# Performance work log

Measured on AMD Instinct MI355X. Metric: run time of the kernel, lower is better.

The kernel has to match this reference:

```python
import jax, jax.numpy as jnp
import numpy as np

N, Z, E, M0, M1, D = 16384, 100, 400, 4000, 2000, 4


def setup_inputs() -> dict:
    key = jax.random.key(0)
    k = jax.random.split(key, 7)
    return {
        "theta": jax.random.normal(k[0], (N, Z), jnp.float32),
        "alpha0": jax.random.normal(k[1], (M0, E), jnp.float32),
        "alpha1": jax.random.normal(k[2], (M1, E), jnp.float32),
        "beta": jax.random.normal(k[3], (Z, E), jnp.float32),
        "bias0": jax.random.normal(k[4], (D, M0), jnp.float32),
        "bias1": jax.random.normal(k[5], (D, M1), jnp.float32),
        "domain_idx": jax.random.randint(k[6], (N,), 0, D, dtype=jnp.int32),
    }


def _recon_mod(theta, alpha, beta, bias, domain_idx):
    # Topic_mod = (alpha @ beta.T).T == beta @ alpha.T : (Z, M)
    topic = beta @ alpha.T
    # per-domain GEMM + indexed bias-add + log_softmax + scatter-back
    # == single GEMM with per-row gathered bias (all domains present)
    logits = theta @ topic + bias[domain_idx]  # (N, M)
    return jax.nn.log_softmax(logits, axis=-1)


def reference(theta, alpha0, alpha1, beta, bias0, bias1, domain_idx):
    r0 = _recon_mod(theta, alpha0, beta, bias0, domain_idx)
    r1 = _recon_mod(theta, alpha1, beta, bias1, domain_idx)
    return (r0, r1)
```

## Files before the change

### kernel.cpp

```cpp
#include <hip/hip_runtime.h>
#include <hip/hip_bf16.h>

#define PN 16384
#define PZ 100
#define PE 400
#define PM0 4000
#define PM1 2000
#define KP 128
#define SEG1ROW 4096
#define MROWS 6144

typedef __attribute__((ext_vector_type(8))) _Float16 half8v;
typedef __attribute__((ext_vector_type(4))) float floatx4;
typedef __attribute__((ext_vector_type(4))) unsigned int uint4v;

__global__ __launch_bounds__(256) void fill_kernel(uint4v* __restrict__ p, int n16)
{
    int i = blockIdx.x * 256 + threadIdx.x;
    if (i < n16) p[i] = (uint4v){0u, 0u, 0u, 0u};
}

__global__ __launch_bounds__(256) void topic_kernel(
    const float* __restrict__ alpha0, const float* __restrict__ alpha1,
    const float* __restrict__ beta, _Float16* __restrict__ b2t)
{
    __shared__ float sAl[64][101];
    __shared__ float sBt[20][100];

    const int seg = (blockIdx.x >= 64);
    const int tile = seg ? (blockIdx.x - 64) : blockIdx.x;
    const float* alpha = seg ? alpha1 : alpha0;
    const int Mse = seg ? PM1 : PM0;
    const int rowbase = (seg ? SEG1ROW : 0) + tile * 64;
    const int m0 = tile * 64;

    const int tid = threadIdx.x;
    const int ml = tid & 63;
    const int zt = tid >> 6;
    const int z0 = blockIdx.y * 20;

    float acc[5] = {0.f, 0.f, 0.f, 0.f, 0.f};

    for (int ec = 0; ec < 4; ++ec) {
        #pragma unroll
        for (int l = 0; l < 25; ++l) {
            int idx = tid + l * 256;
            int mr = idx / 100;
            int e  = idx - mr * 100;
            int mm = m0 + mr;
            sAl[mr][e] = (mm < Mse) ? alpha[(size_t)mm * PE + ec * 100 + e] : 0.f;
        }
        for (int idx = tid; idx < 2000; idx += 256) {
            int zr = idx / 100;
            int e  = idx - zr * 100;
            sBt[zr][e] = beta[(size_t)(z0 + zr) * PE + ec * 100 + e];
        }
        __syncthreads();

        #pragma unroll 2
        for (int e = 0; e < 100; ++e) {
            float a = sAl[ml][e];
            #pragma unroll
            for (int zi = 0; zi < 5; ++zi)
                acc[zi] = fmaf(sBt[zt * 5 + zi][e], a, acc[zi]);
        }
        __syncthreads();
    }

    int m = m0 + ml;
    if (m < Mse) {
        #pragma unroll
        for (int zi = 0; zi < 5; ++zi)
            b2t[(size_t)(rowbase + ml) * KP + (z0 + zt * 5 + zi)] = (_Float16)acc[zi];
    }
}

__global__ __launch_bounds__(256) void bias_kernel(
    const float* __restrict__ bias0, const float* __restrict__ bias1,
    _Float16* __restrict__ b2t)
{
    int row = blockIdx.x * 256 + threadIdx.x;
    if (row >= MROWS) return;
    int seg = (row >= SEG1ROW);
    int m = row - (seg ? SEG1ROW : 0);
    int Mse = seg ? PM1 : PM0;
    const float* bias = seg ? bias1 : bias0;
    if (m < Mse) {
        #pragma unroll
        for (int d = 0; d < 4; ++d)
            b2t[(size_t)row * KP + 100 + d] = (_Float16)bias[(size_t)d * Mse + m];
    }
}

__global__ __launch_bounds__(512, 4) void fused_kernel(
    const float* __restrict__ theta,
    const _Float16* __restrict__ B2T,
    const int* __restrict__ dom,
    float* __restrict__ out0, float* __restrict__ out1)
{
    __shared__ __align__(1024) char sA[32 * 256];
    __shared__ float smx[8][32];
    __shared__ float sms[8][32];
    __shared__ float slse[32];

    const int tid = threadIdx.x;
    const int w   = tid >> 6;
    const int ll  = tid & 63;
    const int g   = ll >> 4;
    const int c   = ll & 15;
    const int n0  = blockIdx.x * 32;

    {
        int row  = tid >> 4;
        int slot = tid & 15;
        const float* tr = theta + (size_t)(n0 + row) * PZ + slot * 8;
        half8v h = (half8v)(_Float16)0.f;
        if (slot < 12) {
            float4 lo = *(const float4*)tr;
            float4 hi = *(const float4*)(tr + 4);
            h[0] = (_Float16)lo.x; h[1] = (_Float16)lo.y;
            h[2] = (_Float16)lo.z; h[3] = (_Float16)lo.w;
            h[4] = (_Float16)hi.x; h[5] = (_Float16)hi.y;
            h[6] = (_Float16)hi.z; h[7] = (_Float16)hi.w;
        } else if (slot == 12) {
            float4 lo = *(const float4*)tr;
            h[0] = (_Float16)lo.x; h[1] = (_Float16)lo.y;
            h[2] = (_Float16)lo.z; h[3] = (_Float16)lo.w;
            int d = dom[n0 + row];
            h[4] = (_Float16)(d == 0 ? 1.f : 0.f);
            h[5] = (_Float16)(d == 1 ? 1.f : 0.f);
            h[6] = (_Float16)(d == 2 ? 1.f : 0.f);
            h[7] = (_Float16)(d == 3 ? 1.f : 0.f);
        }
        *(half8v*)(sA + row * 256 + ((slot ^ (row & 7)) * 16)) = h;
    }
    __syncthreads();

    half8v aF[2][4];
    #pragma unroll
    for (int mi = 0; mi < 2; ++mi) {
        int row = mi * 16 + c;
        #pragma unroll
        for (int kb = 0; kb < 4; ++kb) {
            int slot = (kb * 4 + g) ^ (row & 7);
            aF[mi][kb] = *(const half8v*)(sA + row * 256 + slot * 16);
        }
    }

    const int mbase = w * 16 + c;

    for (int seg = 0; seg < 2; ++seg) {
        const int Mse = seg ? PM1 : PM0;
        const int NT  = seg ? 16 : 32;
        const _Float16* Bseg = B2T + (size_t)(seg ? SEG1ROW : 0) * KP;
        float* out = seg ? out1 : out0;

        const _Float16* bp0 = Bseg + (size_t)mbase * KP;
        const size_t TSTEP = (size_t)128 * KP;

        float mx_[2][4], sm_[2][4];
        #pragma unroll
        for (int mi = 0; mi < 2; ++mi)
            #pragma unroll
            for (int i = 0; i < 4; ++i) { mx_[mi][i] = -3.0e38f; sm_[mi][i] = 0.f; }

        auto loadB = [&](half8v (&bf)[4], const _Float16* p) {
            #pragma unroll
            for (int kb = 0; kb < 4; ++kb)
                bf[kb] = *(const half8v*)(p + kb * 32 + g * 8);
        };
        auto mfma8 = [&](half8v (&bf)[4], floatx4& a0, floatx4& a1) {
            a0 = (floatx4){0.f, 0.f, 0.f, 0.f};
            a1 = (floatx4){0.f, 0.f, 0.f, 0.f};
            #pragma unroll
            for (int kb = 0; kb < 4; ++kb) {
                a0 = __builtin_amdgcn_mfma_f32_16x16x32_f16(aF[0][kb], bf[kb], a0, 0, 0, 0);
                a1 = __builtin_amdgcn_mfma_f32_16x16x32_f16(aF[1][kb], bf[kb], a1, 0, 0, 0);
            }
        };
        auto stats_step = [&](floatx4& a0, floatx4& a1, int t) {
            const bool mv = (t * 128 + mbase) < Mse;
            float vv[2][4];
            float gm = -3.0e38f;
            #pragma unroll
            for (int mi = 0; mi < 2; ++mi)
                #pragma unroll
                for (int i = 0; i < 4; ++i) {
                    float v = mv ? (mi ? a1[i] : a0[i]) : -1.0e30f;
                    vv[mi][i] = v;
                    gm = fmaxf(gm, v - mx_[mi][i]);
                }
            if (gm <= 8.0f) {
                #pragma unroll
                for (int mi = 0; mi < 2; ++mi)
                    #pragma unroll
                    for (int i = 0; i < 4; ++i)
                        sm_[mi][i] += __expf(vv[mi][i] - mx_[mi][i]);
            } else {
                #pragma unroll
                for (int mi = 0; mi < 2; ++mi)
                    #pragma unroll
                    for (int i = 0; i < 4; ++i) {
                        float v  = vv[mi][i];
                        float nm = fmaxf(mx_[mi][i], v);
                        sm_[mi][i] = sm_[mi][i] * __expf(mx_[mi][i] - nm) + __expf(v - nm);
                        mx_[mi][i] = nm;
                    }
            }
        };

        {
            half8v bA[4], bB[4];
            floatx4 a0, a1;
            const _Float16* bp = bp0;
            loadB(bA, bp);
            for (int t = 0; t < NT; t += 2) {
                loadB(bB, bp + TSTEP);
                mfma8(bA, a0, a1);
                stats_step(a0, a1, t);
                if (t + 2 < NT) loadB(bA, bp + 2 * TSTEP);
                mfma8(bB, a0, a1);
                stats_step(a0, a1, t + 1);
                bp += 2 * TSTEP;
            }
        }

        #pragma unroll
        for (int mi = 0; mi < 2; ++mi) {
            #pragma unroll
            for (int i = 0; i < 4; ++i) {
                float m_ = mx_[mi][i], s_ = sm_[mi][i];
                #pragma unroll
                for (int msk = 1; msk < 16; msk <<= 1) {
                    float mo = __shfl_xor(m_, msk);
                    float so = __shfl_xor(s_, msk);
                    float nm = fmaxf(m_, mo);
                    s_ = s_ * __expf(m_ - nm) + so * __expf(mo - nm);
                    m_ = nm;
                }
                if (c == 0) {
                    int row = mi * 16 + 4 * g + i;
                    smx[w][row] = m_;
                    sms[w][row] = s_;
                }
            }
        }
        __syncthreads();
        if (tid < 32) {
            float m_ = smx[0][tid], s_ = sms[0][tid];
            #pragma unroll
            for (int wv = 1; wv < 8; ++wv) {
                float mo = smx[wv][tid];
                float so = sms[wv][tid];
                float nm = fmaxf(m_, mo);
                s_ = s_ * __expf(m_ - nm) + so * __expf(mo - nm);
                m_ = nm;
            }
            slse[tid] = m_ + __logf(s_);
        }
        __syncthreads();
        float lse_[2][4];
        #pragma unroll
        for (int mi = 0; mi < 2; ++mi)
            #pragma unroll
            for (int i = 0; i < 4; ++i)
                lse_[mi][i] = slse[mi * 16 + 4 * g + i];
        __syncthreads();

        {
            float* op[2][4];
            #pragma unroll
            for (int mi = 0; mi < 2; ++mi)
                #pragma unroll
                for (int i = 0; i < 4; ++i)
                    op[mi][i] = out + (size_t)(n0 + mi * 16 + 4 * g + i) * Mse + mbase;

            auto write_step = [&](floatx4& a0, floatx4& a1, int t) {
                const bool mv = (t * 128 + mbase) < Mse;
                if (mv) {
                    #pragma unroll
                    for (int mi = 0; mi < 2; ++mi)
                        #pragma unroll
                        for (int i = 0; i < 4; ++i) {
                            float o = (mi ? a1[i] : a0[i]) - lse_[mi][i];
                            __builtin_nontemporal_store(o, op[mi][i]);
                        }
                }
                #pragma unroll
                for (int mi = 0; mi < 2; ++mi)
                    #pragma unroll
                    for (int i = 0; i < 4; ++i)
                        op[mi][i] += 128;
            };

            half8v bA[4], bB[4];
            floatx4 a0, a1;
            const _Float16* bp = bp0;
            loadB(bA, bp);
            for (int t = 0; t < NT; t += 2) {
                loadB(bB, bp + TSTEP);
                mfma8(bA, a0, a1);
                write_step(a0, a1, t);
                if (t + 2 < NT) loadB(bA, bp + 2 * TSTEP);
                mfma8(bB, a0, a1);
                write_step(a0, a1, t + 1);
                bp += 2 * TSTEP;
            }
        }
    }
}

extern "C" void kernel_launch(void* const* d_in, const int* in_sizes, int n_in,
                              void* d_out, int out_size, void* d_ws, size_t ws_size,
                              hipStream_t stream) {
    const float* theta  = (const float*)d_in[0];
    const float* alpha0 = (const float*)d_in[1];
    const float* alpha1 = (const float*)d_in[2];
    const float* beta   = (const float*)d_in[3];
    const float* bias0  = (const float*)d_in[4];
    const float* bias1  = (const float*)d_in[5];
    const int*   dom    = (const int*)d_in[6];

    float* out0 = (float*)d_out;
    float* out1 = out0 + (size_t)PN * PM0;

    _Float16* B2T = (_Float16*)d_ws;

    {
        int n16 = MROWS * KP * 2 / 16;
        fill_kernel<<<(n16 + 255) / 256, 256, 0, stream>>>((uint4v*)B2T, n16);
    }

    topic_kernel<<<dim3(96, 5), 256, 0, stream>>>(alpha0, alpha1, beta, B2T);

    bias_kernel<<<MROWS / 256, 256, 0, stream>>>(bias0, bias1, B2T);

    fused_kernel<<<PN / 32, 512, 0, stream>>>(theta, B2T, dom, out0, out1);
}
```

Measured before the change: 261.7 us.

## Swap MFMA operands so each lane holds four consecutive columns for vector stores

Swaps the A and B operands of the MFMA so the accumulator is transposed: each lane now owns one output row and four consecutive output columns instead of four rows and one column. This turns the eight scalar nontemporal stores per step into two 16-byte vector stores. It also shrinks the online softmax state from 16 to 4 registers per lane, makes the rescale branch wave-uniform via __all, and cuts the cross-lane reduction to two shuffle steps. The stores are now regular rather than nontemporal, and one barrier is dropped; whether the dropped barrier is safe depends on how slse is reused.

```diff
diff --git a/kernel.cpp b/kernel.cpp
--- a/kernel.cpp
+++ b/kernel.cpp
@@ -147,7 +147,7 @@
         }
     }
 
-    const int mbase = w * 16 + c;
+    const int mwave = w * 16 + 4 * g;
 
     for (int seg = 0; seg < 2; ++seg) {
         const int Mse = seg ? PM1 : PM0;
@@ -155,14 +155,10 @@
         const _Float16* Bseg = B2T + (size_t)(seg ? SEG1ROW : 0) * KP;
         float* out = seg ? out1 : out0;
 
-        const _Float16* bp0 = Bseg + (size_t)mbase * KP;
+        const _Float16* bp0 = Bseg + (size_t)(w * 16 + c) * KP;
         const size_t TSTEP = (size_t)128 * KP;
 
-        float mx_[2][4], sm_[2][4];
-        #pragma unroll
-        for (int mi = 0; mi < 2; ++mi)
-            #pragma unroll
-            for (int i = 0; i < 4; ++i) { mx_[mi][i] = -3.0e38f; sm_[mi][i] = 0.f; }
+        float mx0 = -3.0e38f, mx1 = -3.0e38f, sm0 = 0.f, sm1 = 0.f;
 
         auto loadB = [&](half8v (&bf)[4], const _Float16* p) {
             #pragma unroll
@@ -174,38 +170,36 @@
             a1 = (floatx4){0.f, 0.f, 0.f, 0.f};
             #pragma unroll
             for (int kb = 0; kb < 4; ++kb) {
-                a0 = __builtin_amdgcn_mfma_f32_16x16x32_f16(aF[0][kb], bf[kb], a0, 0, 0, 0);
-                a1 = __builtin_amdgcn_mfma_f32_16x16x32_f16(aF[1][kb], bf[kb], a1, 0, 0, 0);
+                a0 = __builtin_amdgcn_mfma_f32_16x16x32_f16(bf[kb], aF[0][kb], a0, 0, 0, 0);
+                a1 = __builtin_amdgcn_mfma_f32_16x16x32_f16(bf[kb], aF[1][kb], a1, 0, 0, 0);
             }
         };
         auto stats_step = [&](floatx4& a0, floatx4& a1, int t) {
-            const bool mv = (t * 128 + mbase) < Mse;
-            float vv[2][4];
-            float gm = -3.0e38f;
-            #pragma unroll
-            for (int mi = 0; mi < 2; ++mi)
-                #pragma unroll
-                for (int i = 0; i < 4; ++i) {
-                    float v = mv ? (mi ? a1[i] : a0[i]) : -1.0e30f;
-                    vv[mi][i] = v;
-                    gm = fmaxf(gm, v - mx_[mi][i]);
-                }
-            if (gm <= 8.0f) {
-                #pragma unroll
-                for (int mi = 0; mi < 2; ++mi)
-                    #pragma unroll
-                    for (int i = 0; i < 4; ++i)
-                        sm_[mi][i] += __expf(vv[mi][i] - mx_[mi][i]);
+            const bool mval = (t * 128 + mwave) < Mse;
+            float v0[4], v1[4];
+            #pragma unroll
+            for (int i = 0; i < 4; ++i) {
+                v0[i] = mval ? a0[i] : -1.0e30f;
+                v1[i] = mval ? a1[i] : -1.0e30f;
+            }
+            float tm0 = fmaxf(fmaxf(v0[0], v0[1]), fmaxf(v0[2], v0[3]));
+            float tm1 = fmaxf(fmaxf(v1[0], v1[1]), fmaxf(v1[2], v1[3]));
+            float gm = fmaxf(tm0 - mx0, tm1 - mx1);
+            if (__all(gm <= 8.0f)) {
+                sm0 += __expf(v0[0] - mx0) + __expf(v0[1] - mx0)
+                     + __expf(v0[2] - mx0) + __expf(v0[3] - mx0);
+                sm1 += __expf(v1[0] - mx1) + __expf(v1[1] - mx1)
+                     + __expf(v1[2] - mx1) + __expf(v1[3] - mx1);
             } else {
-                #pragma unroll
-                for (int mi = 0; mi < 2; ++mi)
-                    #pragma unroll
-                    for (int i = 0; i < 4; ++i) {
-                        float v  = vv[mi][i];
-                        float nm = fmaxf(mx_[mi][i], v);
-                        sm_[mi][i] = sm_[mi][i] * __expf(mx_[mi][i] - nm) + __expf(v - nm);
-                        mx_[mi][i] = nm;
-                    }
+                float nm0 = fmaxf(mx0, tm0);
+                float nm1 = fmaxf(mx1, tm1);
+                sm0 = sm0 * __expf(mx0 - nm0)
+                    + __expf(v0[0] - nm0) + __expf(v0[1] - nm0)
+                    + __expf(v0[2] - nm0) + __expf(v0[3] - nm0);
+                sm1 = sm1 * __expf(mx1 - nm1)
+                    + __expf(v1[0] - nm1) + __expf(v1[1] - nm1)
+                    + __expf(v1[2] - nm1) + __expf(v1[3] - nm1);
+                mx0 = nm0; mx1 = nm1;
             }
         };
 
@@ -225,24 +219,22 @@
             }
         }
 
-        #pragma unroll
-        for (int mi = 0; mi < 2; ++mi) {
-            #pragma unroll
-            for (int i = 0; i < 4; ++i) {
-                float m_ = mx_[mi][i], s_ = sm_[mi][i];
-                #pragma unroll
-                for (int msk = 1; msk < 16; msk <<= 1) {
-                    float mo = __shfl_xor(m_, msk);
-                    float so = __shfl_xor(s_, msk);
-                    float nm = fmaxf(m_, mo);
-                    s_ = s_ * __expf(m_ - nm) + so * __expf(mo - nm);
-                    m_ = nm;
-                }
-                if (c == 0) {
-                    int row = mi * 16 + 4 * g + i;
-                    smx[w][row] = m_;
-                    sms[w][row] = s_;
-                }
+        {
+            float m0 = mx0, s0 = sm0, m1 = mx1, s1 = sm1;
+            #pragma unroll
+            for (int msk = 16; msk <= 32; msk <<= 1) {
+                float mo0 = __shfl_xor(m0, msk), so0 = __shfl_xor(s0, msk);
+                float mo1 = __shfl_xor(m1, msk), so1 = __shfl_xor(s1, msk);
+                float nm0 = fmaxf(m0, mo0);
+                s0 = s0 * __expf(m0 - nm0) + so0 * __expf(mo0 - nm0);
+                m0 = nm0;
+                float nm1 = fmaxf(m1, mo1);
+                s1 = s1 * __expf(m1 - nm1) + so1 * __expf(mo1 - nm1);
+                m1 = nm1;
+            }
+            if (ll < 16) {
+                smx[w][ll] = m0;      sms[w][ll] = s0;
+                smx[w][16 + ll] = m1; sms[w][16 + ll] = s1;
             }
         }
         __syncthreads();
@@ -259,38 +251,22 @@
             slse[tid] = m_ + __logf(s_);
         }
         __syncthreads();
-        float lse_[2][4];
-        #pragma unroll
-        for (int mi = 0; mi < 2; ++mi)
-            #pragma unroll
-            for (int i = 0; i < 4; ++i)
-                lse_[mi][i] = slse[mi * 16 + 4 * g + i];
-        __syncthreads();
+        const float lse0 = slse[c];
+        const float lse1 = slse[16 + c];
 
         {
-            float* op[2][4];
-            #pragma unroll
-            for (int mi = 0; mi < 2; ++mi)
-                #pragma unroll
-                for (int i = 0; i < 4; ++i)
-                    op[mi][i] = out + (size_t)(n0 + mi * 16 + 4 * g + i) * Mse + mbase;
+            float* p0 = out + (size_t)(n0 + c) * Mse + mwave;
+            float* p1 = out + (size_t)(n0 + 16 + c) * Mse + mwave;
 
             auto write_step = [&](floatx4& a0, floatx4& a1, int t) {
-                const bool mv = (t * 128 + mbase) < Mse;
-                if (mv) {
-                    #pragma unroll
-                    for (int mi = 0; mi < 2; ++mi)
-                        #pragma unroll
-                        for (int i = 0; i < 4; ++i) {
-                            float o = (mi ? a1[i] : a0[i]) - lse_[mi][i];
-                            __builtin_nontemporal_store(o, op[mi][i]);
-                        }
+                if ((t * 128 + mwave) < Mse) {
+                    floatx4 o0 = {a0[0] - lse0, a0[1] - lse0, a0[2] - lse0, a0[3] - lse0};
+                    floatx4 o1 = {a1[0] - lse1, a1[1] - lse1, a1[2] - lse1, a1[3] - lse1};
+                    *(floatx4*)p0 = o0;
+                    *(floatx4*)p1 = o1;
                 }
-                #pragma unroll
-                for (int mi = 0; mi < 2; ++mi)
-                    #pragma unroll
-                    for (int i = 0; i < 4; ++i)
-                        op[mi][i] += 128;
+                p0 += 128;
+                p1 += 128;
             };
 
             half8v bA[4], bB[4];
```

After: 269.6 us. 1.03x slower.
